# Performance work log

Measured on AMD Instinct MI355X. Metric: run time of the kernel, lower is better.

The kernel has to match this reference:

```python
import jax, jax.numpy as jnp
import numpy as np

B, S, H = 8, 2048, 2048


def setup_inputs() -> dict:
    key = jax.random.key(0)
    k1, k2, k3 = jax.random.split(key, 3)
    hidden_state = jax.random.normal(k1, (B, S, H), dtype=jnp.float32)
    attention_mask = jnp.ones((B, S), dtype=jnp.int32)
    special_embeddings_mask = jnp.zeros((B, S), dtype=jnp.int32).at[:, 0].set(1)
    # torch samples -log(Exp(1)) == standard Gumbel; pass noise explicitly for determinism
    gumbel_noise = jax.random.gumbel(k2, (B, S, 2), dtype=jnp.float32)
    W = jax.random.normal(k3, (2 * H, 2), dtype=jnp.float32) / np.sqrt(2.0 * H)
    b = jnp.zeros((2,), dtype=jnp.float32)
    return {"hidden_state": hidden_state, "attention_mask": attention_mask,
            "special_embeddings_mask": special_embeddings_mask,
            "gumbel_noise": gumbel_noise, "W": W, "b": b}


def _forward(hidden_state, W, b, gumbel_noise, attention_mask, special_embeddings_mask):
    Bs, Ss, Hs = hidden_state.shape
    mask_b = attention_mask.astype(bool)
    # adjacent pair features [h_i, h_{i+1}], zero stub appended at the last position
    pairs = jnp.concatenate([hidden_state[:, :-1], hidden_state[:, 1:]], axis=-1)
    pairs = jnp.concatenate([pairs, jnp.zeros((Bs, 1, 2 * Hs), pairs.dtype)], axis=1)
    logits = pairs @ W + b  # [B,S,2]
    # hard Gumbel-softmax with straight-through estimator (tau=1, scale=1, invert=False)
    y_soft = jax.nn.softmax(logits + gumbel_noise, axis=-1)
    index = jnp.argmax(y_soft, axis=-1)
    y_hard = jax.nn.one_hot(index, 2, dtype=logits.dtype)
    mm = y_hard - jax.lax.stop_gradient(y_soft) + y_soft
    # special tokens never merge; padded positions contribute nothing
    mm = jnp.where(special_embeddings_mask.astype(bool)[..., None],
                   jnp.asarray([1.0, 0.0], mm.dtype), mm)
    mm = mm * mask_b[..., None].astype(mm.dtype)
    # ---- vectorized run-length merge (replaces the serial per-batch python loop) ----
    idx = jnp.arange(Ss)
    T = jnp.sum(attention_mask, axis=-1).astype(jnp.int32)  # valid token counts [B]
    valid = idx[None, :] < T[:, None]  # [B,S]
    # a position participates in a merge run iff it votes merge and 1 <= i < T-1
    want = (mm[..., 1] > 0.5) & (idx[None, :] >= 1) & (idx[None, :] < (T[:, None] - 1))
    want_prev = jnp.pad(want[:, :-1], ((0, 0), (1, 0)))
    # new output row starts unless position continues an existing merge run
    inc = (valid & (idx[None, :] >= 1) & ~(want & want_prev)).astype(jnp.int32)
    r = jnp.cumsum(inc, axis=-1)  # destination output row for each input position
    v = jnp.where(want, mm[..., 1], mm[..., 0])
    v = jnp.where(idx[None, :] == 0, jnp.asarray(1.0, v.dtype), v)  # transform[:,0,0] = 1
    v = jnp.where(valid, v, jnp.asarray(0.0, v.dtype))
    b_idx = jnp.arange(Bs)[:, None]
    transform = jnp.zeros((Bs, Ss, Ss), hidden_state.dtype).at[b_idx, r, idx[None, :]].add(v)
    counts = jnp.zeros((Bs, Ss), hidden_state.dtype).at[b_idx, r].add(valid.astype(hidden_state.dtype))
    new_len = r[:, -1] + 1  # merged sequence length per row
    merged_attention_mask = (idx[None, :] < new_len[:, None]).astype(hidden_state.dtype)
    merged_special = jnp.zeros((Bs, Ss), hidden_state.dtype).at[:, 0].set(1.0)
    merged_special = merged_special.at[jnp.arange(Bs), new_len - 1].set(1.0)
    merged_hidden = jnp.einsum('bts,bsh->bth', transform, hidden_state)
    return merged_hidden, merged_attention_mask, merged_special, counts, mm, logits


def reference(hidden_state, attention_mask, special_embeddings_mask, gumbel_noise, W, b):
    return _forward(hidden_state, W, b, gumbel_noise, attention_mask, special_embeddings_mask)
```

## Files before the change

kernel.cpp:

```cpp
#include <hip/hip_runtime.h>
#include <math.h>

#define Bq 8
#define Sq 2048
#define Hq 2048
#define BSq (Bq*Sq)
#define K3_ROWS 8

#define OFF_MH  ((size_t)0)
#define OFF_MAM ((size_t)BSq*Hq)
#define OFF_MSP (OFF_MAM + (size_t)BSq)
#define OFF_CNT (OFF_MSP + (size_t)BSq)
#define OFF_MM  (OFF_CNT + (size_t)BSq)
#define OFF_LG  (OFF_MM + (size_t)2*BSq)

#define WS_DOTS 0
#define WS_V    ((size_t)BSq*16)
#define WS_SEG  (WS_V + (size_t)BSq*4)
#define WS_META (WS_SEG + (size_t)BSq*4)

typedef float nfloat4 __attribute__((ext_vector_type(4)));

__device__ inline float4 f4add(float4 a, float4 b) {
  return make_float4(a.x+b.x, a.y+b.y, a.z+b.z, a.w+b.w);
}

__device__ inline void nt_store_f4(float4 v, float4* p) {
  nfloat4 nv;
  nv.x = v.x; nv.y = v.y; nv.z = v.z; nv.w = v.w;
  __builtin_nontemporal_store(nv, (nfloat4*)p);
}

__global__ __launch_bounds__(256) void k1_dots(const float* __restrict__ hid,
                                               const float* __restrict__ Wg,
                                               float4* __restrict__ dots) {
  __shared__ float4 part[4][256];
  const int tid = threadIdx.x;
  const float4* W4 = (const float4*)Wg;
  const float4 wa0 = W4[2*tid],           wa1 = W4[2*tid+1];
  const float4 wa2 = W4[2*(256+tid)],     wa3 = W4[2*(256+tid)+1];
  const float4 wb0 = W4[1024+2*tid],      wb1 = W4[1024+2*tid+1];
  const float4 wb2 = W4[1024+2*(256+tid)],wb3 = W4[1024+2*(256+tid)+1];
  const int base = blockIdx.x * 16;
  for (int tk0 = 0; tk0 < 16; tk0 += 4) {
    #pragma unroll
    for (int j = 0; j < 4; ++j) {
      const float4* hr = (const float4*)(hid + (size_t)(base + tk0 + j) * Hq);
      float4 h0 = hr[tid], h1 = hr[256+tid];
      float d0 = h0.x*wa0.x + h0.y*wa0.z + h0.z*wa1.x + h0.w*wa1.z
               + h1.x*wa2.x + h1.y*wa2.z + h1.z*wa3.x + h1.w*wa3.z;
      float d1 = h0.x*wa0.y + h0.y*wa0.w + h0.z*wa1.y + h0.w*wa1.w
               + h1.x*wa2.y + h1.y*wa2.w + h1.z*wa3.y + h1.w*wa3.w;
      float e0 = h0.x*wb0.x + h0.y*wb0.z + h0.z*wb1.x + h0.w*wb1.z
               + h1.x*wb2.x + h1.y*wb2.z + h1.z*wb3.x + h1.w*wb3.z;
      float e1 = h0.x*wb0.y + h0.y*wb0.w + h0.z*wb1.y + h0.w*wb1.w
               + h1.x*wb2.y + h1.y*wb2.w + h1.z*wb3.y + h1.w*wb3.w;
      part[j][tid] = make_float4(d0, d1, e0, e1);
    }
    __syncthreads();
    const int w = tid >> 6, l = tid & 63;
    float4 s = f4add(f4add(part[w][l], part[w][l+64]),
                     f4add(part[w][l+128], part[w][l+192]));
    #pragma unroll
    for (int off = 32; off > 0; off >>= 1) {
      s.x += __shfl_xor(s.x, off);
      s.y += __shfl_xor(s.y, off);
      s.z += __shfl_xor(s.z, off);
      s.w += __shfl_xor(s.w, off);
    }
    if (l == 0) dots[base + tk0 + w] = s;
    __syncthreads();
  }
}

__global__ __launch_bounds__(256) void k2_merge(const float4* __restrict__ dots,
                                                const int* __restrict__ attn,
                                                const int* __restrict__ spec,
                                                const float* __restrict__ gum,
                                                const float* __restrict__ bias,
                                                float* __restrict__ out,
                                                float* __restrict__ v_ws,
                                                int* __restrict__ seg_ws,
                                                int* __restrict__ meta) {
  const int b = blockIdx.x, tid = threadIdx.x;
  __shared__ int sums[256];
  __shared__ unsigned char wantL[Sq];
  __shared__ int seg[Sq];
  __shared__ int sT;
  const float b0 = bias[0], b1 = bias[1];

  int tsum = 0;
  #pragma unroll
  for (int k = 0; k < 8; ++k) tsum += attn[b*Sq + tid*8 + k];
  sums[tid] = tsum; __syncthreads();
  for (int off = 128; off > 0; off >>= 1) {
    if (tid < off) sums[tid] += sums[tid+off];
    __syncthreads();
  }
  if (tid == 0) sT = sums[0];
  __syncthreads();
  const int T = sT;

  int wloc[8];
  #pragma unroll
  for (int k = 0; k < 8; ++k) {
    const int i  = tid*8 + k;
    const int gi = b*Sq + i;
    float4 di = dots[gi];
    float l0, l1;
    if (i < Sq-1) {
      float4 dn = dots[gi+1];
      l0 = (di.x + dn.z) + b0;
      l1 = (di.y + dn.w) + b1;
    } else { l0 = b0; l1 = b1; }
    out[OFF_LG + (size_t)gi*2 + 0] = l0;
    out[OFF_LG + (size_t)gi*2 + 1] = l1;
    float z0 = l0 + gum[(size_t)gi*2 + 0];
    float z1 = l1 + gum[(size_t)gi*2 + 1];
    float m  = fmaxf(z0, z1);
    float e0 = expf(z0 - m), e1 = expf(z1 - m);
    float den = e0 + e1;
    float p0 = e0 / den, p1 = e1 / den;
    int idx1 = (p1 > p0) ? 1 : 0;
    float h0f = idx1 ? 0.0f : 1.0f, h1f = idx1 ? 1.0f : 0.0f;
    float mm0 = (h0f - p0) + p0;
    float mm1 = (h1f - p1) + p1;
    if (spec[gi] != 0) { mm0 = 1.0f; mm1 = 0.0f; }
    float am = (float)attn[gi];
    mm0 *= am; mm1 *= am;
    out[OFF_MM + (size_t)gi*2 + 0] = mm0;
    out[OFF_MM + (size_t)gi*2 + 1] = mm1;
    int want = (mm1 > 0.5f) && (i >= 1) && (i < T-1);
    wantL[i] = (unsigned char)want;
    wloc[k]  = want;
    float v = want ? mm1 : mm0;
    if (i == 0) v = 1.0f;
    if (i >= T) v = 0.0f;
    v_ws[gi] = v;
  }
  __syncthreads();

  int incs[8]; int run = 0;
  #pragma unroll
  for (int k = 0; k < 8; ++k) {
    const int i = tid*8 + k;
    int wprev = (i >= 1) ? (int)wantL[i-1] : 0;
    int inc = (i < T && i >= 1 && !(wloc[k] && wprev)) ? 1 : 0;
    run += inc;
    incs[k] = run;
  }
  sums[tid] = run; __syncthreads();
  for (int off = 1; off < 256; off <<= 1) {
    int val = (tid >= off) ? sums[tid - off] : 0;
    __syncthreads();
    sums[tid] += val;
    __syncthreads();
  }
  const int excl = sums[tid] - run;
  const int total = sums[255];

  if (tid == 0) seg[0] = 0;
  #pragma unroll
  for (int k = 0; k < 8; ++k) {
    const int i = tid*8 + k;
    int inc = (k == 0) ? incs[0] : (incs[k] - incs[k-1]);
    if (inc) seg[excl + incs[k]] = i;
  }
  __syncthreads();

  const int nl = total + 1;
  if (tid == 0) { meta[b*2] = nl; meta[b*2+1] = T; }

  #pragma unroll
  for (int k = 0; k < 8; ++k) {
    const int t  = tid*8 + k;
    const int gi = b*Sq + t;
    seg_ws[gi] = (t < nl) ? seg[t] : 0;
    float cnt = 0.0f, mam = 0.0f, msp = 0.0f;
    if (t < nl) {
      int s0 = seg[t];
      int s1 = (t+1 < nl) ? seg[t+1] : T;
      cnt = (float)(s1 - s0);
      mam = 1.0f;
    }
    if (t == 0 || t == nl-1) msp = 1.0f;
    out[OFF_MAM + gi] = mam;
    out[OFF_MSP + gi] = msp;
    out[OFF_CNT + gi] = cnt;
  }
}

__global__ __launch_bounds__(256) void k3_gather(const float* __restrict__ hid,
                                                 const float* __restrict__ v_ws,
                                                 const int* __restrict__ seg_ws,
                                                 const int* __restrict__ meta,
                                                 float* __restrict__ out_mh) {
  const int blocksPerBatch = Sq / K3_ROWS;
  const int b  = blockIdx.x / blocksPerBatch;
  const int t0 = (blockIdx.x % blocksPerBatch) * K3_ROWS;
  const int tid = threadIdx.x;
  const int nl = meta[b*2];
  const int T  = meta[b*2+1];

  __shared__ int bound[K3_ROWS + 1];
  if (tid <= K3_ROWS) {
    const int t = t0 + tid;
    bound[tid] = (t < nl) ? seg_ws[b*Sq + t] : T;
  }
  __syncthreads();

  const int rbase = b*Sq;
  const int i0 = bound[0], iN = bound[K3_ROWS];

  const float4 z4 = make_float4(0.f,0.f,0.f,0.f);
  float4 c0 = z4, c1 = z4, n0 = z4, n1 = z4;
  float wc = 0.f, wn = 0.f;
  if (i0 < iN) {
    const float4* hr = (const float4*)(hid + (size_t)(rbase + i0) * Hq);
    c0 = hr[tid]; c1 = hr[256 + tid]; wc = v_ws[rbase + i0];
  }
  if (i0 + 1 < iN) {
    const float4* hr = (const float4*)(hid + (size_t)(rbase + i0 + 1) * Hq);
    n0 = hr[tid]; n1 = hr[256 + tid]; wn = v_ws[rbase + i0 + 1];
  }

  int i = i0, r = 0;
  float4 a0 = z4, a1 = z4;
  while (r < K3_ROWS) {
    while (r < K3_ROWS && i >= bound[r + 1]) {
      float4* orow = (float4*)(out_mh + (size_t)(rbase + t0 + r) * Hq);
      nt_store_f4(a0, orow + tid);
      nt_store_f4(a1, orow + 256 + tid);
      a0 = z4; a1 = z4;
      ++r;
    }
    if (r >= K3_ROWS) break;
    float4 f0 = z4, f1 = z4; float wf = 0.f;
    if (i + 2 < iN) {
      const float4* hr = (const float4*)(hid + (size_t)(rbase + i + 2) * Hq);
      f0 = hr[tid]; f1 = hr[256 + tid]; wf = v_ws[rbase + i + 2];
    }
    a0.x = fmaf(wc, c0.x, a0.x); a0.y = fmaf(wc, c0.y, a0.y);
    a0.z = fmaf(wc, c0.z, a0.z); a0.w = fmaf(wc, c0.w, a0.w);
    a1.x = fmaf(wc, c1.x, a1.x); a1.y = fmaf(wc, c1.y, a1.y);
    a1.z = fmaf(wc, c1.z, a1.z); a1.w = fmaf(wc, c1.w, a1.w);
    c0 = n0; c1 = n1; wc = wn;
    n0 = f0; n1 = f1; wn = wf;
    ++i;
  }
}

extern "C" void kernel_launch(void* const* d_in, const int* in_sizes, int n_in,
                              void* d_out, int out_size, void* d_ws, size_t ws_size,
                              hipStream_t stream) {
  (void)in_sizes; (void)n_in; (void)out_size; (void)ws_size;
  const float* hid  = (const float*)d_in[0];
  const int*   attn = (const int*)d_in[1];
  const int*   spec = (const int*)d_in[2];
  const float* gum  = (const float*)d_in[3];
  const float* Wg   = (const float*)d_in[4];
  const float* bias = (const float*)d_in[5];
  float* out = (float*)d_out;
  char*  ws  = (char*)d_ws;
  float4* dots  = (float4*)(ws + WS_DOTS);
  float* v_ws   = (float*)(ws + WS_V);
  int*   seg_ws = (int*)(ws + WS_SEG);
  int*   meta   = (int*)(ws + WS_META);

  k1_dots<<<dim3(BSq/16), dim3(256), 0, stream>>>(hid, Wg, dots);
  k2_merge<<<dim3(Bq), dim3(256), 0, stream>>>(dots, attn, spec, gum, bias,
                                               out, v_ws, seg_ws, meta);
  k3_gather<<<dim3(Bq*(Sq/K3_ROWS)), dim3(256), 0, stream>>>(hid, v_ws, seg_ws,
                                                             meta, out + OFF_MH);
}
```

Baseline: 272.0 us.

## Fuse three kernels into one persistent launch with atomic counters and flags

```diff
diff --git a/kernel.cpp b/kernel.cpp
--- a/kernel.cpp
+++ b/kernel.cpp
@@ -6,6 +6,9 @@
 #define Hq 2048
 #define BSq (Bq*Sq)
 #define K3_ROWS 8
+#define NK1 (BSq/16)
+#define NK3 (BSq/K3_ROWS)
+#define K1_PER_B (NK1/Bq)
 
 #define OFF_MH  ((size_t)0)
 #define OFF_MAM ((size_t)BSq*Hq)
@@ -18,6 +21,9 @@
 #define WS_V    ((size_t)BSq*16)
 #define WS_SEG  (WS_V + (size_t)BSq*4)
 #define WS_META (WS_SEG + (size_t)BSq*4)
+#define WS_CNT  (WS_META + 64)
+#define WS_FLAG (WS_CNT + 32)
+#define WS_END  (WS_FLAG + 32)
 
 typedef float nfloat4 __attribute__((ext_vector_type(4)));
 
@@ -31,17 +37,18 @@
   __builtin_nontemporal_store(nv, (nfloat4*)p);
 }
 
-__global__ __launch_bounds__(256) void k1_dots(const float* __restrict__ hid,
-                                               const float* __restrict__ Wg,
-                                               float4* __restrict__ dots) {
-  __shared__ float4 part[4][256];
-  const int tid = threadIdx.x;
+
+__device__ inline void phase1_dots(int blk, int tid,
+                                   const float* __restrict__ hid,
+                                   const float* __restrict__ Wg,
+                                   float4* __restrict__ dots,
+                                   float4 (*part)[256]) {
   const float4* W4 = (const float4*)Wg;
   const float4 wa0 = W4[2*tid],           wa1 = W4[2*tid+1];
   const float4 wa2 = W4[2*(256+tid)],     wa3 = W4[2*(256+tid)+1];
   const float4 wb0 = W4[1024+2*tid],      wb1 = W4[1024+2*tid+1];
   const float4 wb2 = W4[1024+2*(256+tid)],wb3 = W4[1024+2*(256+tid)+1];
-  const int base = blockIdx.x * 16;
+  const int base = blk * 16;
   for (int tk0 = 0; tk0 < 16; tk0 += 4) {
     #pragma unroll
     for (int j = 0; j < 4; ++j) {
@@ -73,20 +80,18 @@
   }
 }
 
-__global__ __launch_bounds__(256) void k2_merge(const float4* __restrict__ dots,
-                                                const int* __restrict__ attn,
-                                                const int* __restrict__ spec,
-                                                const float* __restrict__ gum,
-                                                const float* __restrict__ bias,
-                                                float* __restrict__ out,
-                                                float* __restrict__ v_ws,
-                                                int* __restrict__ seg_ws,
-                                                int* __restrict__ meta) {
-  const int b = blockIdx.x, tid = threadIdx.x;
-  __shared__ int sums[256];
-  __shared__ unsigned char wantL[Sq];
-  __shared__ int seg[Sq];
-  __shared__ int sT;
+__device__ inline void phase2_merge(int b, int tid,
+                                    const float4* __restrict__ dots,
+                                    const int* __restrict__ attn,
+                                    const int* __restrict__ spec,
+                                    const float* __restrict__ gum,
+                                    const float* __restrict__ bias,
+                                    float* __restrict__ out,
+                                    float* __restrict__ v_ws,
+                                    int* __restrict__ seg_ws,
+                                    int* __restrict__ meta,
+                                    int* sums, unsigned char* wantL, int* seg,
+                                    int* sTp) {
   const float b0 = bias[0], b1 = bias[1];
 
   int tsum = 0;
@@ -97,9 +102,9 @@
     if (tid < off) sums[tid] += sums[tid+off];
     __syncthreads();
   }
-  if (tid == 0) sT = sums[0];
+  if (tid == 0) *sTp = sums[0];
   __syncthreads();
-  const int T = sT;
+  const int T = *sTp;
 
   int wloc[8];
   #pragma unroll
@@ -190,19 +195,19 @@
   }
 }
 
-__global__ __launch_bounds__(256) void k3_gather(const float* __restrict__ hid,
-                                                 const float* __restrict__ v_ws,
-                                                 const int* __restrict__ seg_ws,
-                                                 const int* __restrict__ meta,
-                                                 float* __restrict__ out_mh) {
+__device__ inline void phase3_gather(int k3blk, int tid,
+                                     const float* __restrict__ hid,
+                                     const float* __restrict__ v_ws,
+                                     const int* __restrict__ seg_ws,
+                                     const int* __restrict__ meta,
+                                     float* __restrict__ out_mh,
+                                     int* bound) {
   const int blocksPerBatch = Sq / K3_ROWS;
-  const int b  = blockIdx.x / blocksPerBatch;
-  const int t0 = (blockIdx.x % blocksPerBatch) * K3_ROWS;
-  const int tid = threadIdx.x;
+  const int b  = k3blk / blocksPerBatch;
+  const int t0 = (k3blk % blocksPerBatch) * K3_ROWS;
   const int nl = meta[b*2];
   const int T  = meta[b*2+1];
 
-  __shared__ int bound[K3_ROWS + 1];
   if (tid <= K3_ROWS) {
     const int t = t0 + tid;
     bound[tid] = (t < nl) ? seg_ws[b*Sq + t] : T;
@@ -250,10 +255,94 @@
   }
 }
 
+__global__ __launch_bounds__(256) void fused_pc(
+    const float* __restrict__ hid, const int* __restrict__ attn,
+    const int* __restrict__ spec, const float* __restrict__ gum,
+    const float* __restrict__ Wg, const float* __restrict__ bias,
+    float* __restrict__ out, float4* __restrict__ dots,
+    float* __restrict__ v_ws, int* __restrict__ seg_ws,
+    int* __restrict__ meta, int* __restrict__ cnt, int* __restrict__ flag) {
+  __shared__ __align__(16) char smem[16384];
+  __shared__ int bound[K3_ROWS + 1];
+  __shared__ int lastFlag;
+  const int blk = blockIdx.x, tid = threadIdx.x;
+
+  if (blk < NK1) {
+    const int b = blk / K1_PER_B;
+    phase1_dots(blk, tid, hid, Wg, dots, (float4 (*)[256])smem);
+    __syncthreads();
+    __threadfence();
+    if (tid == 0) {
+      int old = __hip_atomic_fetch_add(&cnt[b], 1, __ATOMIC_ACQ_REL,
+                                       __HIP_MEMORY_SCOPE_AGENT);
+      lastFlag = (old == K1_PER_B - 1);
+    }
+    __syncthreads();
+    if (lastFlag) {
+      __threadfence();
+      int* sums            = (int*)smem;
+      unsigned char* wantL = (unsigned char*)(smem + 1024);
+      int* seg             = (int*)(smem + 1024 + 2048);
+      int* sTp             = (int*)(smem + 1024 + 2048 + 8192);
+      phase2_merge(b, tid, dots, attn, spec, gum, bias, out,
+                   v_ws, seg_ws, meta, sums, wantL, seg, sTp);
+      __syncthreads();
+      __threadfence();
+      if (tid == 0)
+        __hip_atomic_store(&flag[b], 1, __ATOMIC_RELEASE,
+                           __HIP_MEMORY_SCOPE_AGENT);
+    }
+  } else {
+    const int k3blk = blk - NK1;
+    const int b = k3blk / (Sq / K3_ROWS);
+    if (tid == 0) {
+      while (__hip_atomic_load(&flag[b], __ATOMIC_ACQUIRE,
+                               __HIP_MEMORY_SCOPE_AGENT) == 0)
+        __builtin_amdgcn_s_sleep(8);
+    }
+    __syncthreads();
+    __threadfence();
+    phase3_gather(k3blk, tid, hid, v_ws, seg_ws, meta, out + OFF_MH, bound);
+  }
+}
+
+__global__ __launch_bounds__(256) void k1_dots(const float* __restrict__ hid,
+                                               const float* __restrict__ Wg,
+                                               float4* __restrict__ dots) {
+  __shared__ float4 part[4][256];
+  phase1_dots(blockIdx.x, threadIdx.x, hid, Wg, dots, part);
+}
+
+__global__ __launch_bounds__(256) void k2_merge(const float4* __restrict__ dots,
+                                                const int* __restrict__ attn,
+                                                const int* __restrict__ spec,
+                                                const float* __restrict__ gum,
+                                                const float* __restrict__ bias,
+                                                float* __restrict__ out,
+                                                float* __restrict__ v_ws,
+                                                int* __restrict__ seg_ws,
+                                                int* __restrict__ meta) {
+  __shared__ int sums[256];
+  __shared__ unsigned char wantL[Sq];
+  __shared__ int seg[Sq];
+  __shared__ int sT;
+  phase2_merge(blockIdx.x, threadIdx.x, dots, attn, spec, gum, bias, out,
+               v_ws, seg_ws, meta, sums, wantL, seg, &sT);
+}
+
+__global__ __launch_bounds__(256) void k3_gather(const float* __restrict__ hid,
+                                                 const float* __restrict__ v_ws,
+                                                 const int* __restrict__ seg_ws,
+                                                 const int* __restrict__ meta,
+                                                 float* __restrict__ out_mh) {
+  __shared__ int bound[K3_ROWS + 1];
+  phase3_gather(blockIdx.x, threadIdx.x, hid, v_ws, seg_ws, meta, out_mh, bound);
+}
+
 extern "C" void kernel_launch(void* const* d_in, const int* in_sizes, int n_in,
                               void* d_out, int out_size, void* d_ws, size_t ws_size,
                               hipStream_t stream) {
-  (void)in_sizes; (void)n_in; (void)out_size; (void)ws_size;
+  (void)in_sizes; (void)n_in; (void)out_size;
   const float* hid  = (const float*)d_in[0];
   const int*   attn = (const int*)d_in[1];
   const int*   spec = (const int*)d_in[2];
@@ -266,10 +355,19 @@
   float* v_ws   = (float*)(ws + WS_V);
   int*   seg_ws = (int*)(ws + WS_SEG);
   int*   meta   = (int*)(ws + WS_META);
-
-  k1_dots<<<dim3(BSq/16), dim3(256), 0, stream>>>(hid, Wg, dots);
-  k2_merge<<<dim3(Bq), dim3(256), 0, stream>>>(dots, attn, spec, gum, bias,
-                                               out, v_ws, seg_ws, meta);
-  k3_gather<<<dim3(Bq*(Sq/K3_ROWS)), dim3(256), 0, stream>>>(hid, v_ws, seg_ws,
-                                                             meta, out + OFF_MH);
-}
+  int*   cnt    = (int*)(ws + WS_CNT);
+  int*   flag   = (int*)(ws + WS_FLAG);
+
+  if (ws_size >= WS_END) {
+    hipMemsetAsync(ws + WS_CNT, 0, 64, stream);
+    fused_pc<<<dim3(NK1 + NK3), dim3(256), 0, stream>>>(
+        hid, attn, spec, gum, Wg, bias, out, dots, v_ws, seg_ws, meta,
+        cnt, flag);
+  } else {
+    k1_dots<<<dim3(NK1), dim3(256), 0, stream>>>(hid, Wg, dots);
+    k2_merge<<<dim3(Bq), dim3(256), 0, stream>>>(dots, attn, spec, gum, bias,
+                                                 out, v_ws, seg_ws, meta);
+    k3_gather<<<dim3(NK3), dim3(256), 0, stream>>>(hid, v_ws, seg_ws,
+                                                   meta, out + OFF_MH);
+  }
+}
```

Result: slower. 934.8 us (+243.7%).
